# Kernel tuning notes

Measured on AMD Instinct MI355X. Metric: run time of the kernel, lower is better.

Reference implementation:

```python
import jax, jax.numpy as jnp
import numpy as np

VARIATION_SCALE = 0.05
TEMPORAL_SMOOTHING = 0.9
TEMPERATURE = 1.0
N_PATTERNS = 8


def setup_inputs() -> dict:
    key = jax.random.key(0)
    k_x, k_w, k_p, k_n = jax.random.split(key, 4)
    B, T, H = 4, 8192, 1024
    return {
        "x": jax.random.normal(k_x, (B, T, H), jnp.float32),
        "W_sel": jax.random.normal(k_w, (H, N_PATTERNS), jnp.float32) * 0.02,
        "b_sel": jnp.zeros((N_PATTERNS,), jnp.float32),
        "patterns": jax.random.normal(k_p, (N_PATTERNS, H), jnp.float32) * 0.1,
        "noise": jax.random.normal(k_n, (B, T, H), jnp.float32),
    }


def reference(x, W_sel, b_sel, patterns, noise):
    # pattern mixture: softmax over 8 learned patterns, per token
    logits = (jnp.einsum("bth,hp->btp", x, W_sel) + b_sel) * TEMPERATURE  # [B,T,8]
    pattern_weights = jax.nn.softmax(logits, axis=-1)
    variation = jnp.einsum("btp,ph->bth", pattern_weights, patterns)  # [B,T,H]

    # EMA noise recurrence: state_t = s*state_{t-1} + (1-s)*eps_t, state_0 = 0
    eps = noise * (VARIATION_SCALE * TEMPERATURE)  # [B,T,H]

    def step(carry, e_t):
        c = TEMPORAL_SMOOTHING * carry + (1.0 - TEMPORAL_SMOOTHING) * e_t
        return c, c

    init = jnp.zeros((x.shape[0], x.shape[2]), x.dtype)  # [B,H]
    _, states = jax.lax.scan(step, init, jnp.swapaxes(eps, 0, 1))  # [T,B,H]
    states = jnp.swapaxes(states, 0, 1)  # [B,T,H]

    return x + variation + states
```

## Files before the change

kernel.cpp:

```cpp
#include <hip/hip_runtime.h>


#define T_LEN 8192
#define H_DIM 1024
#define B_DIM 4
#define NPAT 8
#define CHUNK 128
#define WARM 64
#define NCHUNK (T_LEN / CHUNK)
#define HSPLIT 4
#define HSL (H_DIM / HSPLIT)

static_assert(WARM < CHUNK, "warm-up must stay within previous chunk");

__global__ __launch_bounds__(256) void kA_weights(
    const float* __restrict__ x, const float* __restrict__ Wsel,
    const float* __restrict__ bsel, float* __restrict__ wts)
{
    const int wave = threadIdx.x >> 6;
    const int lane = threadIdx.x & 63;
    const int tok0 = blockIdx.x * 8 + wave * 2;
    const float* x0 = x + (size_t)tok0 * H_DIM;
    const float* x1 = x0 + H_DIM;

    float a0[NPAT], a1[NPAT];
#pragma unroll
    for (int p = 0; p < NPAT; ++p) { a0[p] = 0.0f; a1[p] = 0.0f; }

#pragma unroll
    for (int r = 0; r < 16; ++r) {
        const int h = r * 64 + lane;
        const float4 wa = *(const float4*)(Wsel + (size_t)h * NPAT);
        const float4 wb = *(const float4*)(Wsel + (size_t)h * NPAT + 4);
        const float v0 = x0[h];
        const float v1 = x1[h];
        a0[0] = fmaf(v0, wa.x, a0[0]);  a1[0] = fmaf(v1, wa.x, a1[0]);
        a0[1] = fmaf(v0, wa.y, a0[1]);  a1[1] = fmaf(v1, wa.y, a1[1]);
        a0[2] = fmaf(v0, wa.z, a0[2]);  a1[2] = fmaf(v1, wa.z, a1[2]);
        a0[3] = fmaf(v0, wa.w, a0[3]);  a1[3] = fmaf(v1, wa.w, a1[3]);
        a0[4] = fmaf(v0, wb.x, a0[4]);  a1[4] = fmaf(v1, wb.x, a1[4]);
        a0[5] = fmaf(v0, wb.y, a0[5]);  a1[5] = fmaf(v1, wb.y, a1[5]);
        a0[6] = fmaf(v0, wb.z, a0[6]);  a1[6] = fmaf(v1, wb.z, a1[6]);
        a0[7] = fmaf(v0, wb.w, a0[7]);  a1[7] = fmaf(v1, wb.w, a1[7]);
    }

#pragma unroll
    for (int off = 1; off < 64; off <<= 1) {
#pragma unroll
        for (int p = 0; p < NPAT; ++p) {
            a0[p] += __shfl_xor(a0[p], off, 64);
            a1[p] += __shfl_xor(a1[p], off, 64);
        }
    }

#pragma unroll
    for (int p = 0; p < NPAT; ++p) {
        a0[p] += bsel[p];
        a1[p] += bsel[p];
    }

    float m0 = a0[0], m1 = a1[0];
#pragma unroll
    for (int p = 1; p < NPAT; ++p) { m0 = fmaxf(m0, a0[p]); m1 = fmaxf(m1, a1[p]); }
    float e0[NPAT], e1[NPAT], s0 = 0.0f, s1 = 0.0f;
#pragma unroll
    for (int p = 0; p < NPAT; ++p) {
        e0[p] = __expf(a0[p] - m0); s0 += e0[p];
        e1[p] = __expf(a1[p] - m1); s1 += e1[p];
    }
    const float i0 = 1.0f / s0, i1 = 1.0f / s1;

    if (lane == 0) {
        float* wp = wts + (size_t)tok0 * NPAT;
        *(float4*)(wp + 0)  = make_float4(e0[0]*i0, e0[1]*i0, e0[2]*i0, e0[3]*i0);
        *(float4*)(wp + 4)  = make_float4(e0[4]*i0, e0[5]*i0, e0[6]*i0, e0[7]*i0);
        *(float4*)(wp + 8)  = make_float4(e1[0]*i1, e1[1]*i1, e1[2]*i1, e1[3]*i1);
        *(float4*)(wp + 12) = make_float4(e1[4]*i1, e1[5]*i1, e1[6]*i1, e1[7]*i1);
    }
}

__global__ __launch_bounds__(256) void kB_fused(
    const float* __restrict__ x, const float* __restrict__ noise,
    const float* __restrict__ patterns, const float* __restrict__ wts,
    float* __restrict__ out)
{
    __shared__ float wsm[CHUNK * NPAT];

    const int cid = blockIdx.x;
    const int hs  = cid & (HSPLIT - 1);
    const int bc  = cid >> 2;
    const int b   = bc / NCHUNK;
    const int c   = bc % NCHUNK;
    const int t0  = c * CHUNK;
    const size_t tokbase = (size_t)b * T_LEN + t0;
    const int tid = threadIdx.x;
    const int h   = hs * HSL + tid;

    *(float4*)(wsm + tid * 4) = *(const float4*)(wts + tokbase * NPAT + tid * 4);
    __syncthreads();

    float pat[NPAT];
#pragma unroll
    for (int p = 0; p < NPAT; ++p)
        pat[p] = patterns[p * H_DIM + h];

    float s = 0.0f;
    const int nw = (c == 0) ? 0 : WARM;
    const float* nptr = noise + (tokbase - nw) * (size_t)H_DIM + h;
#pragma unroll 4
    for (int i = 0; i < nw; ++i) {
        s = fmaf(0.9f, s, 0.005f * (*nptr));
        nptr += H_DIM;
    }

    const float* xptr = x + tokbase * H_DIM + h;
    float*       optr = out + tokbase * H_DIM + h;
#pragma unroll 4
    for (int i = 0; i < CHUNK; ++i) {
        const float nv = *nptr;
        const float xv = *xptr;
        s = fmaf(0.9f, s, 0.005f * nv);

        const float4 wA = *(const float4*)(wsm + i * NPAT);
        const float4 wB = *(const float4*)(wsm + i * NPAT + 4);
        float v = 0.0f;
        v = fmaf(wA.x, pat[0], v);
        v = fmaf(wA.y, pat[1], v);
        v = fmaf(wA.z, pat[2], v);
        v = fmaf(wA.w, pat[3], v);
        v = fmaf(wB.x, pat[4], v);
        v = fmaf(wB.y, pat[5], v);
        v = fmaf(wB.z, pat[6], v);
        v = fmaf(wB.w, pat[7], v);

        *optr = xv + v + s;
        nptr += H_DIM; xptr += H_DIM; optr += H_DIM;
    }
}

extern "C" void kernel_launch(void* const* d_in, const int* in_sizes, int n_in,
                              void* d_out, int out_size, void* d_ws, size_t ws_size,
                              hipStream_t stream) {
    const float* x        = (const float*)d_in[0];
    const float* Wsel     = (const float*)d_in[1];
    const float* bsel     = (const float*)d_in[2];
    const float* patterns = (const float*)d_in[3];
    const float* noise    = (const float*)d_in[4];
    float* out = (float*)d_out;
    float* wts = (float*)d_ws;

    const int n_tok = B_DIM * T_LEN;
    kA_weights<<<n_tok / 8, 256, 0, stream>>>(x, Wsel, bsel, wts);
    kB_fused<<<B_DIM * NCHUNK * HSPLIT, 256, 0, stream>>>(x, noise, patterns, wts, out);
}
```

Before: 356.0 us.

## Process 8 tokens per wave in logits kernel and halve recurrence chunk size

```diff
diff --git a/kernel.cpp b/kernel.cpp
--- a/kernel.cpp
+++ b/kernel.cpp
@@ -5,13 +5,13 @@
 #define H_DIM 1024
 #define B_DIM 4
 #define NPAT 8
-#define CHUNK 128
+#define CHUNK 64
 #define WARM 64
 #define NCHUNK (T_LEN / CHUNK)
 #define HSPLIT 4
 #define HSL (H_DIM / HSPLIT)
 
-static_assert(WARM < CHUNK, "warm-up must stay within previous chunk");
+static_assert(WARM <= CHUNK, "warm-up must stay within previous chunk");
 
 __global__ __launch_bounds__(256) void kA_weights(
     const float* __restrict__ x, const float* __restrict__ Wsel,
@@ -19,64 +19,64 @@
 {
     const int wave = threadIdx.x >> 6;
     const int lane = threadIdx.x & 63;
-    const int tok0 = blockIdx.x * 8 + wave * 2;
-    const float* x0 = x + (size_t)tok0 * H_DIM;
-    const float* x1 = x0 + H_DIM;
+    const int tok0 = blockIdx.x * 32 + wave * 8;
 
-    float a0[NPAT], a1[NPAT];
+    float a[64];
 #pragma unroll
-    for (int p = 0; p < NPAT; ++p) { a0[p] = 0.0f; a1[p] = 0.0f; }
+    for (int q = 0; q < 64; ++q) a[q] = 0.0f;
 
-#pragma unroll
+    const float* xbase = x + (size_t)tok0 * H_DIM + lane;
+
+#pragma unroll 2
     for (int r = 0; r < 16; ++r) {
         const int h = r * 64 + lane;
         const float4 wa = *(const float4*)(Wsel + (size_t)h * NPAT);
         const float4 wb = *(const float4*)(Wsel + (size_t)h * NPAT + 4);
-        const float v0 = x0[h];
-        const float v1 = x1[h];
-        a0[0] = fmaf(v0, wa.x, a0[0]);  a1[0] = fmaf(v1, wa.x, a1[0]);
-        a0[1] = fmaf(v0, wa.y, a0[1]);  a1[1] = fmaf(v1, wa.y, a1[1]);
-        a0[2] = fmaf(v0, wa.z, a0[2]);  a1[2] = fmaf(v1, wa.z, a1[2]);
-        a0[3] = fmaf(v0, wa.w, a0[3]);  a1[3] = fmaf(v1, wa.w, a1[3]);
-        a0[4] = fmaf(v0, wb.x, a0[4]);  a1[4] = fmaf(v1, wb.x, a1[4]);
-        a0[5] = fmaf(v0, wb.y, a0[5]);  a1[5] = fmaf(v1, wb.y, a1[5]);
-        a0[6] = fmaf(v0, wb.z, a0[6]);  a1[6] = fmaf(v1, wb.z, a1[6]);
-        a0[7] = fmaf(v0, wb.w, a0[7]);  a1[7] = fmaf(v1, wb.w, a1[7]);
-    }
-
+        float xv[8];
 #pragma unroll
-    for (int off = 1; off < 64; off <<= 1) {
+        for (int j = 0; j < 8; ++j)
+            xv[j] = xbase[(size_t)j * H_DIM + r * 64];
 #pragma unroll
-        for (int p = 0; p < NPAT; ++p) {
-            a0[p] += __shfl_xor(a0[p], off, 64);
-            a1[p] += __shfl_xor(a1[p], off, 64);
+        for (int j = 0; j < 8; ++j) {
+            a[j * 8 + 0] = fmaf(xv[j], wa.x, a[j * 8 + 0]);
+            a[j * 8 + 1] = fmaf(xv[j], wa.y, a[j * 8 + 1]);
+            a[j * 8 + 2] = fmaf(xv[j], wa.z, a[j * 8 + 2]);
+            a[j * 8 + 3] = fmaf(xv[j], wa.w, a[j * 8 + 3]);
+            a[j * 8 + 4] = fmaf(xv[j], wb.x, a[j * 8 + 4]);
+            a[j * 8 + 5] = fmaf(xv[j], wb.y, a[j * 8 + 5]);
+            a[j * 8 + 6] = fmaf(xv[j], wb.z, a[j * 8 + 6]);
+            a[j * 8 + 7] = fmaf(xv[j], wb.w, a[j * 8 + 7]);
         }
     }
 
 #pragma unroll
-    for (int p = 0; p < NPAT; ++p) {
-        a0[p] += bsel[p];
-        a1[p] += bsel[p];
+    for (int s = 0; s < 6; ++s) {
+        const int o = 1 << s;
+        const int half = 32 >> s;
+        const bool hib = (lane & o) != 0;
+#pragma unroll
+        for (int m = 0; m < half; ++m) {
+            const float lo = a[2 * m];
+            const float hi = a[2 * m + 1];
+            const float disc = hib ? lo : hi;
+            const float keep = hib ? hi : lo;
+            a[m] = keep + __shfl_xor(disc, o, 64);
+        }
     }
 
-    float m0 = a0[0], m1 = a1[0];
-#pragma unroll
-    for (int p = 1; p < NPAT; ++p) { m0 = fmaxf(m0, a0[p]); m1 = fmaxf(m1, a1[p]); }
-    float e0[NPAT], e1[NPAT], s0 = 0.0f, s1 = 0.0f;
-#pragma unroll
-    for (int p = 0; p < NPAT; ++p) {
-        e0[p] = __expf(a0[p] - m0); s0 += e0[p];
-        e1[p] = __expf(a1[p] - m1); s1 += e1[p];
-    }
-    const float i0 = 1.0f / s0, i1 = 1.0f / s1;
+    const float logit = a[0] + bsel[lane & 7];
 
-    if (lane == 0) {
-        float* wp = wts + (size_t)tok0 * NPAT;
-        *(float4*)(wp + 0)  = make_float4(e0[0]*i0, e0[1]*i0, e0[2]*i0, e0[3]*i0);
-        *(float4*)(wp + 4)  = make_float4(e0[4]*i0, e0[5]*i0, e0[6]*i0, e0[7]*i0);
-        *(float4*)(wp + 8)  = make_float4(e1[0]*i1, e1[1]*i1, e1[2]*i1, e1[3]*i1);
-        *(float4*)(wp + 12) = make_float4(e1[4]*i1, e1[5]*i1, e1[6]*i1, e1[7]*i1);
-    }
+    float mx = logit;
+    mx = fmaxf(mx, __shfl_xor(mx, 1, 64));
+    mx = fmaxf(mx, __shfl_xor(mx, 2, 64));
+    mx = fmaxf(mx, __shfl_xor(mx, 4, 64));
+    const float e = __expf(logit - mx);
+    float sum = e;
+    sum += __shfl_xor(sum, 1, 64);
+    sum += __shfl_xor(sum, 2, 64);
+    sum += __shfl_xor(sum, 4, 64);
+
+    wts[(size_t)tok0 * NPAT + lane] = e / sum;
 }
 
 __global__ __launch_bounds__(256) void kB_fused(
@@ -89,14 +89,14 @@
     const int cid = blockIdx.x;
     const int hs  = cid & (HSPLIT - 1);
     const int bc  = cid >> 2;
-    const int b   = bc / NCHUNK;
-    const int c   = bc % NCHUNK;
+    const int b   = bc >> 7;
+    const int c   = bc & (NCHUNK - 1);
     const int t0  = c * CHUNK;
     const size_t tokbase = (size_t)b * T_LEN + t0;
     const int tid = threadIdx.x;
     const int h   = hs * HSL + tid;
 
-    *(float4*)(wsm + tid * 4) = *(const float4*)(wts + tokbase * NPAT + tid * 4);
+    *(float2*)(wsm + tid * 2) = *(const float2*)(wts + tokbase * NPAT + tid * 2);
     __syncthreads();
 
     float pat[NPAT];
@@ -107,7 +107,7 @@
     float s = 0.0f;
     const int nw = (c == 0) ? 0 : WARM;
     const float* nptr = noise + (tokbase - nw) * (size_t)H_DIM + h;
-#pragma unroll 4
+#pragma unroll 8
     for (int i = 0; i < nw; ++i) {
         s = fmaf(0.9f, s, 0.005f * (*nptr));
         nptr += H_DIM;
@@ -115,7 +115,7 @@
 
     const float* xptr = x + tokbase * H_DIM + h;
     float*       optr = out + tokbase * H_DIM + h;
-#pragma unroll 4
+#pragma unroll 8
     for (int i = 0; i < CHUNK; ++i) {
         const float nv = *nptr;
         const float xv = *xptr;
@@ -150,6 +150,6 @@
     float* wts = (float*)d_ws;
 
     const int n_tok = B_DIM * T_LEN;
-    kA_weights<<<n_tok / 8, 256, 0, stream>>>(x, Wsel, bsel, wts);
+    kA_weights<<<n_tok / 32, 256, 0, stream>>>(x, Wsel, bsel, wts);
     kB_fused<<<B_DIM * NCHUNK * HSPLIT, 256, 0, stream>>>(x, noise, patterns, wts, out);
 }
```

Result: slower. 376.3 us (+5.7%).
